# Optimization experiments

Measured on AMD Instinct MI355X. Metric: run time of the kernel, lower is better.

The kernel has to match this reference:

```python
import jax, jax.numpy as jnp
import numpy as np

IN_FEATURES = 256
OUT_FEATURES = 256
INTERNAL = (IN_FEATURES + OUT_FEATURES) // 2  # trajectron AdditiveAttention default


def setup_inputs() -> dict:
    key = jax.random.key(0)
    k1, k2, k3, k4, k5 = jax.random.split(key, 5)
    B, TH, TQ = 32, 256, 64
    inputs = jax.random.normal(k1, (B, TH, IN_FEATURES), dtype=jnp.float32)
    state = jax.random.normal(k2, (B, TQ, OUT_FEATURES), dtype=jnp.float32)
    # Linear weights (no bias), Kaiming-ish scale
    w1 = jax.random.normal(k3, (INTERNAL, IN_FEATURES), dtype=jnp.float32) / np.sqrt(IN_FEATURES)
    w2 = jax.random.normal(k4, (INTERNAL, OUT_FEATURES), dtype=jnp.float32) / np.sqrt(OUT_FEATURES)
    v = jax.random.normal(k5, (INTERNAL,), dtype=jnp.float32) / np.sqrt(INTERNAL)
    return {"inputs": inputs, "state": state, "w1": w1, "w2": w2, "v": v, "batch_size": B}


def reference(inputs, state, w1, w2, v, batch_size):
    # history annotations: (B, Th, Din); future annotations (queries): (B, Tq, Dout)
    keys = inputs.reshape(batch_size, -1, IN_FEATURES)
    queries = state.reshape(batch_size, -1, OUT_FEATURES)
    # Additive (Bahdanau) attention: score = v . tanh(W1 k + W2 q)
    k_proj = jnp.einsum('bti,di->btd', keys, w1)       # (B, Th, D)
    q_proj = jnp.einsum('bqo,do->bqd', queries, w2)    # (B, Tq, D)
    scores = jnp.einsum('d,bqtd->bqt', v, jnp.tanh(q_proj[:, :, None, :] + k_proj[:, None, :, :]))
    alpha = jax.nn.softmax(scores, axis=-1)            # softmax over history axis
    contexts = jnp.einsum('bqt,bti->bqi', alpha, keys)  # (B, Tq, Din)
    # reshape + dropout (eval mode / p effectively 0 -> identity)
    return contexts.reshape(-1, IN_FEATURES)
```

## Files before the change

### kernel.cpp

```cpp
#include <hip/hip_runtime.h>
#include <math.h>

#define BATCH 32
#define TH    256
#define TQn   64
#define DIN   256
#define DD    256
#define QT    4
#define E2C   2.885390081777927f

typedef __attribute__((ext_vector_type(8)))  short bf16x8;
typedef __attribute__((ext_vector_type(16))) float floatx16;
typedef __attribute__((ext_vector_type(4)))  float f32x4;

__device__ __forceinline__ float eclamp(float x) {
    return __builtin_amdgcn_exp2f(fminf(x * E2C, 30.f));
}

__device__ __forceinline__ void split2(float x0, float x1, unsigned& hi, unsigned& lo) {
    unsigned u0 = __float_as_uint(x0), u1 = __float_as_uint(x1);
    unsigned h0 = u0 & 0xFFFF0000u,   h1 = u1 & 0xFFFF0000u;
    float r0 = x0 - __uint_as_float(h0);
    float r1 = x1 - __uint_as_float(h1);
    hi = (u0 >> 16) | h1;
    lo = (__float_as_uint(r0) >> 16) | (__float_as_uint(r1) & 0xFFFF0000u);
}

__device__ __forceinline__ void split8(float4 f0, float4 f1, uint4& hi, uint4& lo) {
    split2(f0.x, f0.y, hi.x, lo.x);
    split2(f0.z, f0.w, hi.y, lo.y);
    split2(f1.x, f1.y, hi.z, lo.z);
    split2(f1.z, f1.w, hi.w, lo.w);
}

#define REG4  65
#define WOFF  (16 * REG4)
#define TSTR  68
__global__ __launch_bounds__(256, 4)
void proj_kernel(const float* __restrict__ keys,
                 const float* __restrict__ state,
                 const float* __restrict__ w1,
                 const float* __restrict__ w2,
                 float* __restrict__ ktp,
                 float* __restrict__ qpo)
{
    __shared__ uint4 lds4[2 * 16 * REG4];

    const int bid = blockIdx.x;
    const int tid = threadIdx.x;

    const float* X;
    const float* W;
    int m0, n0;
    bool is_kp;
    if (bid < 512) {
        is_kp = true;
        m0 = (bid >> 2) * 64;
        n0 = (bid & 3) * 64;
        X = keys; W = w1;
    } else {
        is_kp = false;
        int lb = bid - 512;
        m0 = (lb >> 2) * 64;
        n0 = (lb & 3) * 64;
        X = state; W = w2;
    }

    const int w    = tid >> 6;
    const int l    = tid & 63;
    const int mt   = w >> 1;
    const int nt   = w & 1;
    const int srow = tid >> 3;
    const int kg   = tid & 7;
    const int s_s  = kg >> 1;
    const int lidx = (srow & 31) + 32 * (kg & 1);

    floatx16 acc = {};

    for (int k0 = 0; k0 < DIN; k0 += 64) {
        #pragma unroll
        for (int hrow = 0; hrow < 2; hrow++) {
            int m = srow + hrow * 32;
            const float* px = X + (size_t)(m0 + m) * DIN + k0 + kg * 8;
            uint4 hi, lo;
            split8(*(const float4*)px, *(const float4*)(px + 4), hi, lo);
            int g = m >> 5;
            lds4[((0 * 2 + g) * 4 + s_s) * REG4 + lidx] = hi;
            lds4[((2 + g) * 4 + s_s) * REG4 + lidx] = lo;
            const float* pw = W + (size_t)(n0 + m) * DIN + k0 + kg * 8;
            split8(*(const float4*)pw, *(const float4*)(pw + 4), hi, lo);
            lds4[WOFF + ((0 * 2 + g) * 4 + s_s) * REG4 + lidx] = hi;
            lds4[WOFF + ((2 + g) * 4 + s_s) * REG4 + lidx] = lo;
        }
        __syncthreads();

        #pragma unroll
        for (int s = 0; s < 4; s++) {
            uint4 ahr = lds4[((0 * 2 + mt) * 4 + s) * REG4 + l];
            uint4 alr = lds4[((2 + mt) * 4 + s) * REG4 + l];
            uint4 bhr = lds4[WOFF + ((0 * 2 + nt) * 4 + s) * REG4 + l];
            uint4 blr = lds4[WOFF + ((2 + nt) * 4 + s) * REG4 + l];
            bf16x8 ah = __builtin_bit_cast(bf16x8, ahr);
            bf16x8 al = __builtin_bit_cast(bf16x8, alr);
            bf16x8 bh = __builtin_bit_cast(bf16x8, bhr);
            bf16x8 bl = __builtin_bit_cast(bf16x8, blr);
            acc = __builtin_amdgcn_mfma_f32_32x32x16_bf16(ah, bh, acc, 0, 0, 0);
            acc = __builtin_amdgcn_mfma_f32_32x32x16_bf16(al, bh, acc, 0, 0, 0);
            acc = __builtin_amdgcn_mfma_f32_32x32x16_bf16(ah, bl, acc, 0, 0, 0);
        }
        __syncthreads();
    }

    const int col = l & 31;
    const int hl  = l >> 5;
    if (is_kp) {
        float* sT = (float*)lds4;
        const int d_local = nt * 32 + col;
        #pragma unroll
        for (int r = 0; r < 16; r++) {
            int t_local = mt * 32 + 4 * hl + 8 * (r >> 2) + (r & 3);
            sT[t_local * TSTR + d_local] = eclamp(acc[r]);
        }
        __syncthreads();
        const int b  = m0 >> 8;
        const int t0 = m0 & 255;
        float4* dst4 = (float4*)ktp;
        #pragma unroll
        for (int p = 0; p < 4; p++) {
            int dp_local = w * 4 + p;
            float4 v4 = *(float4*)&sT[l * TSTR + dp_local * 4];
            dst4[(size_t)(b * 64 + (n0 >> 2) + dp_local) * 256 + t0 + l] = v4;
        }
    } else {
        const int d = n0 + nt * 32 + col;
        #pragma unroll
        for (int r = 0; r < 16; r++) {
            int row = (r & 3) + 8 * (r >> 2) + 4 * hl;
            qpo[(size_t)(m0 + mt * 32 + row) * DD + d] = eclamp(acc[r]);
        }
    }
}

__global__ __launch_bounds__(1024, 8)
void attn_kernel(const float* __restrict__ keys,
                 const float* __restrict__ vvec,
                 const float* __restrict__ ktp,
                 const float* __restrict__ qp,
                 float* __restrict__ out)
{
    __shared__ float s_part[4][QT][TH];
    __shared__ float s_alpha[QT][TH];
    __shared__ float s_rsum[QT];

    const int bid  = blockIdx.x;
    const int b    = bid & 31;
    const int q0   = (bid >> 5) * QT;
    const int tid  = threadIdx.x;
    const int t    = tid & 255;
    const int dgu  = __builtin_amdgcn_readfirstlane(tid >> 8);
    const int lane = tid & 63;
    const int wv   = tid >> 6;

    float acc[QT];
    #pragma unroll
    for (int q = 0; q < QT; q++) acc[q] = 0.f;

    const float4* kb4 = (const float4*)ktp + ((size_t)(b * 64 + dgu * 16) * 256 + t);
    const float* pqr0 = qp + (size_t)(b * TQn + q0 + 0) * DD + dgu * 64;
    const float* pqr1 = qp + (size_t)(b * TQn + q0 + 1) * DD + dgu * 64;
    const float* pqr2 = qp + (size_t)(b * TQn + q0 + 2) * DD + dgu * 64;
    const float* pqr3 = qp + (size_t)(b * TQn + q0 + 3) * DD + dgu * 64;
    const float* vvp  = vvec + dgu * 64;

    float4 kv0 = kb4[0 * 256], kv1 = kb4[1 * 256],
           kv2 = kb4[2 * 256], kv3 = kb4[3 * 256];

    #pragma unroll
    for (int c = 0; c < 4; c++) {
        float4 n0v, n1v, n2v, n3v;
        if (c < 3) {
            const float4* p = kb4 + (size_t)(c + 1) * 4 * 256;
            n0v = p[0 * 256]; n1v = p[1 * 256];
            n2v = p[2 * 256]; n3v = p[3 * 256];
        }
        #pragma unroll
        for (int u = 0; u < 4; u++) {
            const int dp = c * 4 + u;
            float4 kv = (u == 0) ? kv0 : (u == 1) ? kv1 : (u == 2) ? kv2 : kv3;
            const float v0 = vvp[dp * 4 + 0], v1 = vvp[dp * 4 + 1];
            const float v2 = vvp[dp * 4 + 2], v3 = vvp[dp * 4 + 3];
            const float* pqr[QT] = {pqr0, pqr1, pqr2, pqr3};
            #pragma unroll
            for (int q = 0; q < QT; q++) {
                const float* pr = pqr[q];
                float d0 = fmaf(pr[dp * 4 + 0], kv.x, 1.f);
                float d1 = fmaf(pr[dp * 4 + 1], kv.y, 1.f);
                float n01 = fmaf(v1, d0, v0 * d1);
                acc[q] = fmaf(n01, __builtin_amdgcn_rcpf(d0 * d1), acc[q]);
                float d2 = fmaf(pr[dp * 4 + 2], kv.z, 1.f);
                float d3 = fmaf(pr[dp * 4 + 3], kv.w, 1.f);
                float n23 = fmaf(v3, d2, v2 * d3);
                acc[q] = fmaf(n23, __builtin_amdgcn_rcpf(d2 * d3), acc[q]);
            }
        }
        if (c < 3) { kv0 = n0v; kv1 = n1v; kv2 = n2v; kv3 = n3v; }
    }

    #pragma unroll
    for (int q = 0; q < QT; q++) s_part[dgu][q][t] = acc[q];
    __syncthreads();

    if (wv < QT) {
        const int q = wv;
        float x0, x1, x2, x3;
        {
            float p0 = s_part[0][q][lane]       + s_part[1][q][lane]
                     + s_part[2][q][lane]       + s_part[3][q][lane];
            float p1 = s_part[0][q][lane + 64]  + s_part[1][q][lane + 64]
                     + s_part[2][q][lane + 64]  + s_part[3][q][lane + 64];
            float p2 = s_part[0][q][lane + 128] + s_part[1][q][lane + 128]
                     + s_part[2][q][lane + 128] + s_part[3][q][lane + 128];
            float p3 = s_part[0][q][lane + 192] + s_part[1][q][lane + 192]
                     + s_part[2][q][lane + 192] + s_part[3][q][lane + 192];
            x0 = -2.f * p0; x1 = -2.f * p1; x2 = -2.f * p2; x3 = -2.f * p3;
        }
        float m = fmaxf(fmaxf(x0, x1), fmaxf(x2, x3));
        #pragma unroll
        for (int off = 32; off >= 1; off >>= 1) m = fmaxf(m, __shfl_xor(m, off));
        float e0 = __expf(x0 - m), e1 = __expf(x1 - m);
        float e2 = __expf(x2 - m), e3 = __expf(x3 - m);
        s_alpha[q][lane]       = e0;
        s_alpha[q][lane + 64]  = e1;
        s_alpha[q][lane + 128] = e2;
        s_alpha[q][lane + 192] = e3;
        float s = (e0 + e1) + (e2 + e3);
        #pragma unroll
        for (int off = 32; off >= 1; off >>= 1) s += __shfl_xor(s, off);
        if (lane == 0) s_rsum[q] = 1.f / s;
    }
    __syncthreads();

    {
        const int iqg = __builtin_amdgcn_readfirstlane((tid >> 6) & 3);
        const int il  = lane & 15;
        const int tl  = lane >> 4;
        const int iq  = iqg * 16 + il;

        f32x4 ctx4[QT] = {};
        const float* kp0 = keys + ((size_t)b * TH + dgu * 64 + tl) * DIN + iq * 4;

        #pragma unroll 4
        for (int step = 0; step < 16; step++) {
            f32x4 key4 = *(const f32x4*)(kp0 + (size_t)step * 4 * DIN);
            const int ta = dgu * 64 + step * 4 + tl;
            #pragma unroll
            for (int q = 0; q < QT; q++)
                ctx4[q] += key4 * s_alpha[q][ta];
        }

        #pragma unroll
        for (int q = 0; q < QT; q++) {
            #pragma unroll
            for (int k = 0; k < 4; k++) {
                ctx4[q][k] += __shfl_xor(ctx4[q][k], 16);
                ctx4[q][k] += __shfl_xor(ctx4[q][k], 32);
            }
        }
        if (tl == 0) {
            #pragma unroll
            for (int q = 0; q < QT; q++)
                *(f32x4*)&s_part[dgu][q][iq * 4] = ctx4[q];
        }
    }
    __syncthreads();

    if (tid < 256) {
        const int q = tid >> 6, iqf = tid & 63;
        f32x4 s = *(const f32x4*)&s_part[0][q][iqf * 4];
        s += *(const f32x4*)&s_part[1][q][iqf * 4];
        s += *(const f32x4*)&s_part[2][q][iqf * 4];
        s += *(const f32x4*)&s_part[3][q][iqf * 4];
        s *= s_rsum[q];
        *(f32x4*)&out[(size_t)(b * TQn + q0 + q) * DIN + iqf * 4] = s;
    }
}

extern "C" void kernel_launch(void* const* d_in, const int* in_sizes, int n_in,
                              void* d_out, int out_size, void* d_ws, size_t ws_size,
                              hipStream_t stream) {
    (void)in_sizes; (void)n_in; (void)out_size; (void)ws_size;
    const float* keys  = (const float*)d_in[0];
    const float* state = (const float*)d_in[1];
    const float* w1    = (const float*)d_in[2];
    const float* w2    = (const float*)d_in[3];
    const float* v     = (const float*)d_in[4];
    float* out = (float*)d_out;

    float* ktp = (float*)d_ws;
    float* qp  = ktp + (size_t)BATCH * DD * TH;

    hipLaunchKernelGGL(proj_kernel, dim3(640), dim3(256), 0, stream,
                       keys, state, w1, w2, ktp, qp);
    hipLaunchKernelGGL(attn_kernel, dim3(BATCH * (TQn / QT)), dim3(1024), 0, stream,
                       keys, v, ktp, qp, out);
}
```

Baseline: 104.4 us.

## Process eight queries per block and drop softmax max-subtraction

Each attention block now handles eight query rows instead of four, so every transposed key value loaded is reused across twice as many queries, and the block count is halved. The softmax no longer computes the row max and its cross-lane reduction; it takes exp2 of the raw scaled scores directly, which relies on the scores being bounded so nothing overflows. Register pressure per thread rises (eight accumulators, a lower launch-bounds occupancy hint), and there are fewer blocks to fill the GPU.

```diff
diff --git a/kernel.cpp b/kernel.cpp
--- a/kernel.cpp
+++ b/kernel.cpp
@@ -6,8 +6,9 @@
 #define TQn   64
 #define DIN   256
 #define DD    256
-#define QT    4
+#define QT    8
 #define E2C   2.885390081777927f
+#define NL2E  -2.8853900817779268f
 
 typedef __attribute__((ext_vector_type(8)))  short bf16x8;
 typedef __attribute__((ext_vector_type(16))) float floatx16;
@@ -141,7 +142,7 @@
     }
 }
 
-__global__ __launch_bounds__(1024, 8)
+__global__ __launch_bounds__(1024, 4)
 void attn_kernel(const float* __restrict__ keys,
                  const float* __restrict__ vvec,
                  const float* __restrict__ ktp,
@@ -166,11 +167,8 @@
     for (int q = 0; q < QT; q++) acc[q] = 0.f;
 
     const float4* kb4 = (const float4*)ktp + ((size_t)(b * 64 + dgu * 16) * 256 + t);
-    const float* pqr0 = qp + (size_t)(b * TQn + q0 + 0) * DD + dgu * 64;
-    const float* pqr1 = qp + (size_t)(b * TQn + q0 + 1) * DD + dgu * 64;
-    const float* pqr2 = qp + (size_t)(b * TQn + q0 + 2) * DD + dgu * 64;
-    const float* pqr3 = qp + (size_t)(b * TQn + q0 + 3) * DD + dgu * 64;
-    const float* vvp  = vvec + dgu * 64;
+    const float*  pqb = qp + (size_t)(b * TQn + q0) * DD + dgu * 64;
+    const float*  vvp = vvec + dgu * 64;
 
     float4 kv0 = kb4[0 * 256], kv1 = kb4[1 * 256],
            kv2 = kb4[2 * 256], kv3 = kb4[3 * 256];
@@ -189,16 +187,15 @@
             float4 kv = (u == 0) ? kv0 : (u == 1) ? kv1 : (u == 2) ? kv2 : kv3;
             const float v0 = vvp[dp * 4 + 0], v1 = vvp[dp * 4 + 1];
             const float v2 = vvp[dp * 4 + 2], v3 = vvp[dp * 4 + 3];
-            const float* pqr[QT] = {pqr0, pqr1, pqr2, pqr3};
             #pragma unroll
             for (int q = 0; q < QT; q++) {
-                const float* pr = pqr[q];
-                float d0 = fmaf(pr[dp * 4 + 0], kv.x, 1.f);
-                float d1 = fmaf(pr[dp * 4 + 1], kv.y, 1.f);
+                const float* pr = pqb + q * DD + dp * 4;
+                float d0 = fmaf(pr[0], kv.x, 1.f);
+                float d1 = fmaf(pr[1], kv.y, 1.f);
                 float n01 = fmaf(v1, d0, v0 * d1);
                 acc[q] = fmaf(n01, __builtin_amdgcn_rcpf(d0 * d1), acc[q]);
-                float d2 = fmaf(pr[dp * 4 + 2], kv.z, 1.f);
-                float d3 = fmaf(pr[dp * 4 + 3], kv.w, 1.f);
+                float d2 = fmaf(pr[2], kv.z, 1.f);
+                float d3 = fmaf(pr[3], kv.w, 1.f);
                 float n23 = fmaf(v3, d2, v2 * d3);
                 acc[q] = fmaf(n23, __builtin_amdgcn_rcpf(d2 * d3), acc[q]);
             }
@@ -212,23 +209,18 @@
 
     if (wv < QT) {
         const int q = wv;
-        float x0, x1, x2, x3;
-        {
-            float p0 = s_part[0][q][lane]       + s_part[1][q][lane]
-                     + s_part[2][q][lane]       + s_part[3][q][lane];
-            float p1 = s_part[0][q][lane + 64]  + s_part[1][q][lane + 64]
-                     + s_part[2][q][lane + 64]  + s_part[3][q][lane + 64];
-            float p2 = s_part[0][q][lane + 128] + s_part[1][q][lane + 128]
-                     + s_part[2][q][lane + 128] + s_part[3][q][lane + 128];
-            float p3 = s_part[0][q][lane + 192] + s_part[1][q][lane + 192]
-                     + s_part[2][q][lane + 192] + s_part[3][q][lane + 192];
-            x0 = -2.f * p0; x1 = -2.f * p1; x2 = -2.f * p2; x3 = -2.f * p3;
-        }
-        float m = fmaxf(fmaxf(x0, x1), fmaxf(x2, x3));
-        #pragma unroll
-        for (int off = 32; off >= 1; off >>= 1) m = fmaxf(m, __shfl_xor(m, off));
-        float e0 = __expf(x0 - m), e1 = __expf(x1 - m);
-        float e2 = __expf(x2 - m), e3 = __expf(x3 - m);
+        float p0 = s_part[0][q][lane]       + s_part[1][q][lane]
+                 + s_part[2][q][lane]       + s_part[3][q][lane];
+        float p1 = s_part[0][q][lane + 64]  + s_part[1][q][lane + 64]
+                 + s_part[2][q][lane + 64]  + s_part[3][q][lane + 64];
+        float p2 = s_part[0][q][lane + 128] + s_part[1][q][lane + 128]
+                 + s_part[2][q][lane + 128] + s_part[3][q][lane + 128];
+        float p3 = s_part[0][q][lane + 192] + s_part[1][q][lane + 192]
+                 + s_part[2][q][lane + 192] + s_part[3][q][lane + 192];
+        float e0 = __builtin_amdgcn_exp2f(p0 * NL2E);
+        float e1 = __builtin_amdgcn_exp2f(p1 * NL2E);
+        float e2 = __builtin_amdgcn_exp2f(p2 * NL2E);
+        float e3 = __builtin_amdgcn_exp2f(p3 * NL2E);
         s_alpha[q][lane]       = e0;
         s_alpha[q][lane + 64]  = e1;
         s_alpha[q][lane + 128] = e2;
@@ -274,7 +266,7 @@
     }
     __syncthreads();
 
-    if (tid < 256) {
+    if (tid < 512) {
         const int q = tid >> 6, iqf = tid & 63;
         f32x4 s = *(const f32x4*)&s_part[0][q][iqf * 4];
         s += *(const f32x4*)&s_part[1][q][iqf * 4];
```

Measured after the change: 107.5 us. 1.03x slower.
